# Kernel optimization log

Hardware: AMD Instinct MI355X
Metric: run time of the kernel (lower is better)

Reference implementation:

```python
import jax, jax.numpy as jnp
import numpy as np

B, T, H, W = 2, 4, 32, 32
DINO_DIM, COG_DIM, NUM_HEADS = 768, 1920, 12
HEAD_DIM = DINO_DIM // NUM_HEADS


def _layernorm(x, g, b, eps=1e-5):
    mu = jnp.mean(x, axis=-1, keepdims=True)
    var = jnp.mean(jnp.square(x - mu), axis=-1, keepdims=True)
    return (x - mu) * jax.lax.rsqrt(var + eps) * g + b


def setup_inputs() -> dict:
    key = jax.random.key(0)
    ks = jax.random.split(key, 12)
    s_d = 1.0 / np.sqrt(DINO_DIM)
    s_c = 1.0 / np.sqrt(COG_DIM)
    return {
        "dino_query": jax.random.normal(ks[0], (B, DINO_DIM, H, W), jnp.float32),
        "cogvideo_keys": jax.random.normal(ks[1], (B, T, H, W, COG_DIM), jnp.float32),
        "temporal_weights": jax.random.uniform(ks[2], (T,), jnp.float32),
        "Wq": jax.random.normal(ks[3], (DINO_DIM, DINO_DIM), jnp.float32) * s_d,
        "bq": jnp.zeros((DINO_DIM,), jnp.float32),
        "Wk": jax.random.normal(ks[4], (COG_DIM, DINO_DIM), jnp.float32) * s_c,
        "bk": jnp.zeros((DINO_DIM,), jnp.float32),
        "Wv": jax.random.normal(ks[5], (COG_DIM, DINO_DIM), jnp.float32) * s_c,
        "bv": jnp.zeros((DINO_DIM,), jnp.float32),
        "Wo": jax.random.normal(ks[6], (DINO_DIM, DINO_DIM), jnp.float32) * s_d,
        "bo": jnp.zeros((DINO_DIM,), jnp.float32),
        "gq": jnp.ones((DINO_DIM,), jnp.float32),
        "Bq": jnp.zeros((DINO_DIM,), jnp.float32),
        "gkv": jnp.ones((COG_DIM,), jnp.float32),
        "Bkv": jnp.zeros((COG_DIM,), jnp.float32),
    }


def reference(dino_query, cogvideo_keys, temporal_weights,
              Wq, bq, Wk, bk, Wv, bv, Wo, bo, gq, Bq, gkv, Bkv):
    b, c, h, w = dino_query.shape
    t = cogvideo_keys.shape[1]
    hw, tkv = h * w, t * cogvideo_keys.shape[2] * cogvideo_keys.shape[3]

    # [B,C,H,W] -> [B,H,W,C]; project after LayerNorm
    xq = _layernorm(jnp.transpose(dino_query, (0, 2, 3, 1)), gq, Bq)
    xkv = _layernorm(cogvideo_keys, gkv, Bkv)
    q = xq @ Wq + bq                      # [B,H,W,C]
    k = xkv @ Wk + bk                     # [B,T,Hk,Wk,C]
    v = xkv @ Wv + bv

    q = q.reshape(b, hw, NUM_HEADS, HEAD_DIM).transpose(0, 2, 1, 3)    # [B,nh,HW,hd]
    k = k.reshape(b, tkv, NUM_HEADS, HEAD_DIM).transpose(0, 2, 1, 3)   # [B,nh,TKV,hd]
    v = v.reshape(b, tkv, NUM_HEADS, HEAD_DIM).transpose(0, 2, 1, 3)

    scores = jnp.einsum('bnqd,bnkd->bnqk', q, k) / np.sqrt(HEAD_DIM)   # [B,nh,HW,TKV]
    # per-key temporal weight: each of the T frames contributes HW keys
    w_key = jnp.repeat(temporal_weights, tkv // t)                     # [TKV]
    scores = scores * w_key[None, None, None, :]
    probs = jax.nn.softmax(scores, axis=-1)

    out = jnp.einsum('bnqk,bnkd->bnqd', probs, v)                      # [B,nh,HW,hd]
    out = out.transpose(0, 2, 1, 3).reshape(b, h, w, c)
    out = out @ Wo + bo
    return jnp.transpose(out, (0, 3, 1, 2))                            # [B,C,H,W]
```

## Files before the change

### kernel.cpp

```cpp
#include <hip/hip_runtime.h>
#include <hip/hip_bf16.h>
#include <math.h>

#define BB   2
#define HWl  1024
#define DINO 768
#define COG  1920
#define NHh  12
#define TKV  4096
#define MQ   (BB*HWl)
#define MKV  (BB*TKV)
#define NSPL 4
#define ROWS_PER_SPLIT (BB*NHh*HWl)

typedef __attribute__((ext_vector_type(8))) short bf16x8;
typedef __attribute__((ext_vector_type(4))) float f32x4;

__device__ __forceinline__ unsigned short f2bf_bits(float f) {
    __hip_bfloat16 h = __float2bfloat16(f);
    return *reinterpret_cast<unsigned short*>(&h);
}

__device__ __forceinline__ void glds16(const __hip_bfloat16* g, __hip_bfloat16* l) {
    __builtin_amdgcn_global_load_lds((const __attribute__((address_space(1))) void*)g,
                                     (__attribute__((address_space(3))) void*)l, 16, 0, 0);
}

__global__ __launch_bounds__(256) void prep1(const float* __restrict__ dino,
                                             const float* __restrict__ cog,
                                             const float* __restrict__ gkv, const float* __restrict__ Bkv,
                                             const float* __restrict__ Wq, const float* __restrict__ Wk,
                                             const float* __restrict__ Wv, const float* __restrict__ Wo,
                                             float* __restrict__ xqT,
                                             __hip_bfloat16* __restrict__ xkv,
                                             __hip_bfloat16* WqT, __hip_bfloat16* WkvT, __hip_bfloat16* WoT) {
    int bid = blockIdx.x, tid = threadIdx.x;
    if (bid < 2048) {
        const int W = COG, W4 = W >> 2, NC = 8;
        int row = bid * 4 + (tid >> 6), lane = tid & 63;
        const float4* xr = (const float4*)(cog + (size_t)row * W);
        const float4* g4 = (const float4*)gkv;
        const float4* b4 = (const float4*)Bkv;
        float4 v[NC];
        float s = 0.f, ss = 0.f;
        #pragma unroll
        for (int i = 0; i < NC; ++i) {
            int c = lane + i * 64;
            float4 t = (c < W4) ? xr[c] : (float4){0.f, 0.f, 0.f, 0.f};
            v[i] = t;
            s  += t.x + t.y + t.z + t.w;
            ss += t.x * t.x + t.y * t.y + t.z * t.z + t.w * t.w;
        }
        #pragma unroll
        for (int off = 1; off < 64; off <<= 1) {
            s  += __shfl_xor(s, off);
            ss += __shfl_xor(ss, off);
        }
        float mu = s / W;
        float rstd = rsqrtf(ss / W - mu * mu + 1e-5f);
        ushort4* yr = (ushort4*)(xkv + (size_t)row * W);
        #pragma unroll
        for (int i = 0; i < NC; ++i) {
            int c = lane + i * 64;
            if (c < W4) {
                float4 t = v[i];
                float4 gg = g4[c], bb = b4[c];
                ushort4 o;
                o.x = f2bf_bits((t.x - mu) * rstd * gg.x + bb.x);
                o.y = f2bf_bits((t.y - mu) * rstd * gg.y + bb.y);
                o.z = f2bf_bits((t.z - mu) * rstd * gg.z + bb.z);
                o.w = f2bf_bits((t.w - mu) * rstd * gg.w + bb.w);
                yr[c] = o;
            }
        }
    } else if (bid < 2432) {
        int t = bid - 2048;
        int h0 = (t & 15) * 64;
        int c0 = ((t >> 4) % 12) * 64;
        int b = t / 192;
        __shared__ float T[64][65];
        #pragma unroll
        for (int i = 0; i < 16; ++i) {
            int idx = tid + i * 256;
            int c = idx >> 6, h = idx & 63;
            T[c][h] = dino[((size_t)b * DINO + c0 + c) * HWl + h0 + h];
        }
        __syncthreads();
        #pragma unroll
        for (int i = 0; i < 16; ++i) {
            int idx = tid + i * 256;
            int r = idx >> 6, c = idx & 63;
            xqT[((size_t)b * HWl + h0 + r) * DINO + c0 + c] = T[c][r];
        }
    } else {
        int bid2 = bid - 2432;
        int mid = bid2 / 1440, r = bid2 % 1440;
        int k0 = (r % 60) * 32, n0 = (r / 60) * 32;
        const float* src = (mid == 0) ? Wq : (mid == 1) ? Wk : (mid == 2) ? Wv : Wo;
        __hip_bfloat16* dst;
        int rowoff = 0;
        if (mid == 0) dst = WqT;
        else if (mid == 1) dst = WkvT;
        else if (mid == 2) { dst = WkvT; rowoff = 768; }
        else dst = WoT;
        int K = (mid == 1 || mid == 2) ? COG : DINO;
        if (k0 >= K) return;
        __shared__ float T[32][33];
        #pragma unroll
        for (int i = 0; i < 4; ++i) {
            int idx = tid + i * 256;
            int rr = idx >> 5, c = idx & 31;
            T[rr][c] = src[(size_t)(k0 + rr) * DINO + n0 + c];
        }
        __syncthreads();
        #pragma unroll
        for (int i = 0; i < 4; ++i) {
            int idx = tid + i * 256;
            int rr = idx >> 5, c = idx & 31;
            dst[(size_t)(rowoff + n0 + rr) * K + k0 + c] = __float2bfloat16(T[c][rr]);
        }
    }
}

__global__ __launch_bounds__(256) void prep2(const float* __restrict__ x,
                                             const float* __restrict__ g,
                                             const float* __restrict__ be,
                                             __hip_bfloat16* __restrict__ y) {
    const int W = DINO, NC = 3;
    int row = blockIdx.x * 4 + (threadIdx.x >> 6);
    int lane = threadIdx.x & 63;
    const float4* xr = (const float4*)(x + (size_t)row * W);
    const float4* g4 = (const float4*)g;
    const float4* b4 = (const float4*)be;
    float4 v[NC];
    float s = 0.f, ss = 0.f;
    #pragma unroll
    for (int i = 0; i < NC; ++i) {
        int c = lane + i * 64;
        float4 t = xr[c];
        v[i] = t;
        s  += t.x + t.y + t.z + t.w;
        ss += t.x * t.x + t.y * t.y + t.z * t.z + t.w * t.w;
    }
    #pragma unroll
    for (int off = 1; off < 64; off <<= 1) {
        s  += __shfl_xor(s, off);
        ss += __shfl_xor(ss, off);
    }
    float mu = s / W;
    float rstd = rsqrtf(ss / W - mu * mu + 1e-5f);
    ushort4* yr = (ushort4*)(y + (size_t)row * W);
    #pragma unroll
    for (int i = 0; i < NC; ++i) {
        int c = lane + i * 64;
        float4 t = v[i];
        float4 gg = g4[c], bb = b4[c];
        ushort4 o;
        o.x = f2bf_bits((t.x - mu) * rstd * gg.x + bb.x);
        o.y = f2bf_bits((t.y - mu) * rstd * gg.y + bb.y);
        o.z = f2bf_bits((t.z - mu) * rstd * gg.z + bb.z);
        o.w = f2bf_bits((t.w - mu) * rstd * gg.w + bb.w);
        yr[c] = o;
    }
}

#define VM6 asm volatile("s_waitcnt vmcnt(6)" ::: "memory")
#define VM2 asm volatile("s_waitcnt vmcnt(2)" ::: "memory")
#define VM0 asm volatile("s_waitcnt vmcnt(0)" ::: "memory")

#define STAGE_A(d, h, tau) do { \
    int _o = (aRow + (h) * 64) * Kd + (tau) * 64 + cgo; \
    __hip_bfloat16* _dp = SM + (d) * 32768 + (h) * 8192 + wido; \
    glds16(Ag + _o, _dp); \
    glds16(Ag + _o + 128 * Kd, _dp + 4096); \
} while (0)

#define STAGE_B(d, h, tau) do { \
    int _o = (bRow + (h) * 32) * Kd + (tau) * 64 + cgo; \
    __hip_bfloat16* _dp = SM + (d) * 32768 + 16384 + (h) * 8192 + wido; \
    glds16(Bg + _o, _dp); \
    glds16(Bg + _o + 128 * Kd, _dp + 4096); \
} while (0)

#define LDS_A_FRAG(dst, MH) do { \
    const __hip_bfloat16* _Ab = SM + cur * 32768 + (MH) * 8192 + aoff; \
    _Pragma("unroll") \
    for (int i = 0; i < 4; ++i) { \
        dst[i][0] = *(const bf16x8*)(_Ab + i * 1024 + c0); \
        dst[i][1] = *(const bf16x8*)(_Ab + i * 1024 + c1); \
    } \
} while (0)

#define LDS_B_FRAG(dst, NH) do { \
    const __hip_bfloat16* _Bb = SM + cur * 32768 + 16384 + (NH) * 8192 + boff; \
    _Pragma("unroll") \
    for (int j = 0; j < 2; ++j) { \
        dst[j][0] = *(const bf16x8*)(_Bb + j * 1024 + c0); \
        dst[j][1] = *(const bf16x8*)(_Bb + j * 1024 + c1); \
    } \
} while (0)

#define PHASE_MFMA(MH, af) do { \
    __builtin_amdgcn_sched_barrier(0); \
    __builtin_amdgcn_s_barrier(); \
    __builtin_amdgcn_sched_barrier(0); \
    __builtin_amdgcn_s_setprio(1); \
    _Pragma("unroll") \
    for (int i = 0; i < 4; ++i) \
        _Pragma("unroll") \
        for (int j = 0; j < 2; ++j) { \
            f32x4 _t = acc[(MH) * 4 + i][j]; \
            _t = __builtin_amdgcn_mfma_f32_16x16x32_bf16(af[i][0], b0[j][0], _t, 0, 0, 0); \
            _t = __builtin_amdgcn_mfma_f32_16x16x32_bf16(af[i][1], b0[j][1], _t, 0, 0, 0); \
            acc[(MH) * 4 + i][j] = _t; \
        } \
    _Pragma("unroll") \
    for (int i = 0; i < 4; ++i) \
        _Pragma("unroll") \
        for (int j = 0; j < 2; ++j) { \
            f32x4 _t = acc[(MH) * 4 + i][2 + j]; \
            _t = __builtin_amdgcn_mfma_f32_16x16x32_bf16(af[i][0], b1[j][0], _t, 0, 0, 0); \
            _t = __builtin_amdgcn_mfma_f32_16x16x32_bf16(af[i][1], b1[j][1], _t, 0, 0, 0); \
            acc[(MH) * 4 + i][2 + j] = _t; \
        } \
    __builtin_amdgcn_s_setprio(0); \
} while (0)

__global__ __launch_bounds__(512, 2) void stage1(const __hip_bfloat16* __restrict__ xq,
                                                 const __hip_bfloat16* __restrict__ WqT,
                                                 const float* __restrict__ bq,
                                                 __hip_bfloat16* __restrict__ qb,
                                                 const __hip_bfloat16* __restrict__ xkv,
                                                 const __hip_bfloat16* __restrict__ WkvT,
                                                 const float* __restrict__ bk,
                                                 const float* __restrict__ bv,
                                                 __hip_bfloat16* __restrict__ kb,
                                                 __hip_bfloat16* __restrict__ VT) {
    __shared__ __hip_bfloat16 SM[65536];
    int bid = blockIdx.x;
    int tid = threadIdx.x;
    int wid = tid >> 6, lane = tid & 63;
    int l4 = lane & 15, lq = lane >> 4;
    int wr = wid >> 2, wc = wid & 3;
    int tr = tid >> 3;
    int cgo = ((tid & 7) ^ (tr & 7)) * 8;
    int wido = wid * 512;

    const __hip_bfloat16 *Ag, *Bg;
    int m0, n0, Kd, NT, isQ;
    if (bid < 192) {
        int x = bid & 7, i = bid >> 3;
        m0 = (x * 4 + (i & 3)) * 256; n0 = (i >> 2) * 256;
        Ag = xkv; Bg = WkvT; Kd = COG; NT = COG / 64; isQ = 0;
    } else {
        int t = bid - 192;
        m0 = (t & 7) * 256; n0 = (t >> 3) * 256;
        Ag = xq; Bg = WqT; Kd = DINO; NT = DINO / 64; isQ = 1;
    }

    const int aRow = m0 + tr;
    const int bRow = n0 + ((tid >> 8) << 6) + (tr & 31);
    const int aoff = (wr * 64 + l4) * 64;
    const int boff = (wc * 32 + l4) * 64;
    const int c0 = ((lq) ^ (l4 & 7)) * 8;
    const int c1 = ((4 + lq) ^ (l4 & 7)) * 8;

    f32x4 acc[8][4];
    #pragma unroll
    for (int i = 0; i < 8; ++i)
        #pragma unroll
        for (int j = 0; j < 4; ++j) acc[i][j] = (f32x4){0.f, 0.f, 0.f, 0.f};

    bf16x8 a0[4][2], a1[4][2], b0[2][2], b1[2][2];

    STAGE_A(0, 0, 0); STAGE_B(0, 0, 0); STAGE_B(0, 1, 0); STAGE_A(0, 1, 0);
    VM2;
    __builtin_amdgcn_s_barrier();

    for (int g = 0; g < NT; ++g) {
        int cur = g & 1, nxt = cur ^ 1;
        bool s1 = (g + 1 < NT);
        LDS_A_FRAG(a0, 0);
        LDS_B_FRAG(b0, 0);
        LDS_B_FRAG(b1, 1);
        if (s1) { STAGE_A(nxt, 0, g + 1); STAGE_B(nxt, 0, g + 1); STAGE_B(nxt, 1, g + 1); VM6; }
        else VM0;
        PHASE_MFMA(0, a0);
        LDS_A_FRAG(a1, 1);
        if (s1) { STAGE_A(nxt, 1, g + 1); VM2; }
        PHASE_MFMA(1, a1);
    }

    if (isQ) {
        #pragma unroll
        for (int ii = 0; ii < 8; ++ii)
            #pragma unroll
            for (int jj = 0; jj < 4; ++jj) {
                int m = m0 + wr * 128 + (ii >> 2) * 64 + (ii & 3) * 16 + lq * 4;
                int n = n0 + wc * 64 + (jj >> 1) * 32 + (jj & 1) * 16 + l4;
                float bb = bq[n];
                #pragma unroll
                for (int r = 0; r < 4; ++r)
                    qb[(size_t)(m + r) * DINO + n] = __float2bfloat16(acc[ii][jj][r] + bb);
            }
    } else if (n0 < 768) {
        #pragma unroll
        for (int ii = 0; ii < 8; ++ii)
            #pragma unroll
            for (int jj = 0; jj < 4; ++jj) {
                int m = m0 + wr * 128 + (ii >> 2) * 64 + (ii & 3) * 16 + lq * 4;
                int n = n0 + wc * 64 + (jj >> 1) * 32 + (jj & 1) * 16 + l4;
                float bb = bk[n];
                #pragma unroll
                for (int r = 0; r < 4; ++r)
                    kb[(size_t)(m + r) * DINO + n] = __float2bfloat16(acc[ii][jj][r] + bb);
            }
    } else {
        #pragma unroll
        for (int ii = 0; ii < 8; ++ii)
            #pragma unroll
            for (int jj = 0; jj < 4; ++jj) {
                int m = m0 + wr * 128 + (ii >> 2) * 64 + (ii & 3) * 16 + lq * 4;
                int nv = n0 - 768 + wc * 64 + (jj >> 1) * 32 + (jj & 1) * 16 + l4;
                float bb = bv[nv];
                #pragma unroll
                for (int r = 0; r < 4; ++r) {
                    int mm = m + r;
                    VT[((size_t)((mm >> 12) * 768 + nv)) * TKV + (mm & 4095)] =
                        __float2bfloat16(acc[ii][jj][r] + bb);
                }
            }
    }
}

__global__ __launch_bounds__(256) void gemm_o(const __hip_bfloat16* __restrict__ A,
                                              const __hip_bfloat16* __restrict__ Bt,
                                              const float* __restrict__ bias,
                                              float* __restrict__ out) {
    const int K = DINO;
    __shared__ __hip_bfloat16 As[64 * 64];
    __shared__ __hip_bfloat16 Bs[64 * 64];
    int m0 = blockIdx.x * 64, n0 = blockIdx.y * 64;
    int tid = threadIdx.x, w = tid >> 6, lane = tid & 63;
    int l4 = lane & 15, lq = lane >> 4;
    int mq = (w & 1) * 32, nq = (w >> 1) * 32;
    f32x4 acc[2][2];
    #pragma unroll
    for (int i = 0; i < 2; ++i)
        #pragma unroll
        for (int j = 0; j < 2; ++j) acc[i][j] = (f32x4){0.f, 0.f, 0.f, 0.f};

    int rr = tid >> 3;
    int gc = (tid & 7) ^ (rr & 7);
    const __hip_bfloat16* ag = A  + (size_t)(m0 + rr) * K + gc * 8;
    const __hip_bfloat16* bg = Bt + (size_t)(n0 + rr) * K + gc * 8;
    __hip_bfloat16* asl = As + (w * 8) * 64;
    __hip_bfloat16* bsl = Bs + (w * 8) * 64;
    int sws = l4 & 7;

    for (int k0 = 0; k0 < K; k0 += 64) {
        __syncthreads();
        #pragma unroll
        for (int g = 0; g < 2; ++g) {
            glds16(ag + (size_t)(g * 32) * K + k0, asl + g * 32 * 64);
            glds16(bg + (size_t)(g * 32) * K + k0, bsl + g * 32 * 64);
        }
        __syncthreads();
        #pragma unroll
        for (int h = 0; h < 2; ++h) {
            bf16x8 a[2], b[2];
            #pragma unroll
            for (int i = 0; i < 2; ++i)
                a[i] = *(const bf16x8*)(As + (mq + 16 * i + l4) * 64 + (((h * 4 + lq) ^ sws) * 8));
            #pragma unroll
            for (int j = 0; j < 2; ++j)
                b[j] = *(const bf16x8*)(Bs + (nq + 16 * j + l4) * 64 + (((h * 4 + lq) ^ sws) * 8));
            #pragma unroll
            for (int i = 0; i < 2; ++i)
                #pragma unroll
                for (int j = 0; j < 2; ++j)
                    acc[i][j] = __builtin_amdgcn_mfma_f32_16x16x32_bf16(b[j], a[i], acc[i][j], 0, 0, 0);
        }
    }
    #pragma unroll
    for (int i = 0; i < 2; ++i)
        #pragma unroll
        for (int j = 0; j < 2; ++j)
            #pragma unroll
            for (int r = 0; r < 4; ++r) {
                int n = n0 + nq + 16 * j + lq * 4 + r;
                int m = m0 + mq + 16 * i + l4;
                int b = m >> 10, hw = m & 1023;
                out[((size_t)b * DINO + n) * HWl + hw] = acc[i][j][r] + bias[n];
            }
}

__global__ __launch_bounds__(256) void attn4(const __hip_bfloat16* __restrict__ qb,
                                             const __hip_bfloat16* __restrict__ kb,
                                             const __hip_bfloat16* __restrict__ VT,
                                             const float* __restrict__ tw,
                                             __hip_bfloat16* __restrict__ Opart,
                                             float* __restrict__ lpart) {
    int bid = blockIdx.x;
    int g = bid % 96, qc = bid / 96;
    int s = g & 3, bh = g >> 2;
    int head = bh % NHh, b = bh / NHh;
    int tid = threadIdx.x, w = tid >> 6, lane = tid & 63;
    int l4 = lane & 15, lq = lane >> 4;

    __shared__ __hip_bfloat16 Ks[2 * 64 * 64];
    __shared__ __hip_bfloat16 Vs[2 * 64 * 64];
    __shared__ __hip_bfloat16 Ps[4 * 32 * 64];

    const __hip_bfloat16* qbase = qb + (size_t)(b * HWl + qc * 128 + w * 32 + l4) * DINO + head * 64;
    bf16x8 qA0 = *(const bf16x8*)(qbase + lq * 8);
    bf16x8 qA1 = *(const bf16x8*)(qbase + 32 + lq * 8);
    const __hip_bfloat16* qbase2 = qbase + (size_t)16 * DINO;
    bf16x8 qB0 = *(const bf16x8*)(qbase2 + lq * 8);
    bf16x8 qB1 = *(const bf16x8*)(qbase2 + 32 + lq * 8);

    float c = tw[s] * 0.125f * 1.44269504f;
    float l_iA = 0.f, l_iB = 0.f;
    f32x4 oA[4], oB[4];
    #pragma unroll
    for (int j = 0; j < 4; ++j) { oA[j] = (f32x4){0.f,0.f,0.f,0.f}; oB[j] = (f32x4){0.f,0.f,0.f,0.f}; }

    int rowA = w * 16 + (lane >> 3);
    int cg = (lane & 7) ^ ((lane >> 3) & 7);
    const __hip_bfloat16* kg0 = kb + (size_t)(b * TKV + s * 1024 + rowA) * DINO + head * 64 + cg * 8;
    const __hip_bfloat16* kg1 = kg0 + (size_t)8 * DINO;
    const __hip_bfloat16* vg0 = VT + (size_t)(b * 768 + head * 64 + rowA) * TKV + s * 1024 + cg * 8;
    const __hip_bfloat16* vg1 = vg0 + (size_t)8 * TKV;
    int klo0 = (w * 2 + 0) * 512, klo1 = (w * 2 + 1) * 512;

    int sw0 = (lq ^ (l4 & 7)) * 8;
    int sw1 = ((4 + lq) ^ (l4 & 7)) * 8;
    __hip_bfloat16* PsA = Ps + w * 2048 + l4 * 64;
    __hip_bfloat16* PsB = Ps + w * 2048 + (16 + l4) * 64;

    glds16(kg0, Ks + klo0);
    glds16(kg1, Ks + klo1);
    glds16(vg0, Vs + klo0);
    glds16(vg1, Vs + klo1);

    for (int kt = 0; kt < 16; ++kt) {
        int cur = (kt & 1) * 4096;
        __syncthreads();
        if (kt < 15) {
            int nxt = cur ^ 4096;
            glds16(kg0 + (size_t)(kt + 1) * 64 * DINO, Ks + nxt + klo0);
            glds16(kg1 + (size_t)(kt + 1) * 64 * DINO, Ks + nxt + klo1);
            glds16(vg0 + (kt + 1) * 64, Vs + nxt + klo0);
            glds16(vg1 + (kt + 1) * 64, Vs + nxt + klo1);
        }
        const __hip_bfloat16* Kc = Ks + cur;
        const __hip_bfloat16* Vc = Vs + cur;

        f32x4 stA[4], stB[4];
        #pragma unroll
        for (int j = 0; j < 4; ++j) {
            const __hip_bfloat16* kr = Kc + (16 * j + l4) * 64;
            bf16x8 kf0 = *(const bf16x8*)(kr + sw0);
            bf16x8 kf1 = *(const bf16x8*)(kr + sw1);
            f32x4 a = (f32x4){0.f,0.f,0.f,0.f};
            a = __builtin_amdgcn_mfma_f32_16x16x32_bf16(kf0, qA0, a, 0, 0, 0);
            a = __builtin_amdgcn_mfma_f32_16x16x32_bf16(kf1, qA1, a, 0, 0, 0);
            stA[j] = a;
            f32x4 bb = (f32x4){0.f,0.f,0.f,0.f};
            bb = __builtin_amdgcn_mfma_f32_16x16x32_bf16(kf0, qB0, bb, 0, 0, 0);
            bb = __builtin_amdgcn_mfma_f32_16x16x32_bf16(kf1, qB1, bb, 0, 0, 0);
            stB[j] = bb;
        }

        float lsA = 0.f, lsB = 0.f;
        #pragma unroll
        for (int j = 0; j < 4; ++j)
            #pragma unroll
            for (int r = 0; r < 4; ++r) {
                float eA = exp2f(stA[j][r] * c);
                float eB = exp2f(stB[j][r] * c);
                stA[j][r] = eA; lsA += eA;
                stB[j][r] = eB; lsB += eB;
            }
        lsA += __shfl_xor(lsA, 16); lsA += __shfl_xor(lsA, 32);
        lsB += __shfl_xor(lsB, 16); lsB += __shfl_xor(lsB, 32);
        l_iA += lsA; l_iB += lsB;

        #pragma unroll
        for (int j = 0; j < 4; ++j) {
            int off = (((2 * j + (lq >> 1)) ^ (l4 & 7)) << 3) + (lq & 1) * 4;
            ushort4 pA, pB;
            pA.x = f2bf_bits(stA[j][0]); pA.y = f2bf_bits(stA[j][1]);
            pA.z = f2bf_bits(stA[j][2]); pA.w = f2bf_bits(stA[j][3]);
            pB.x = f2bf_bits(stB[j][0]); pB.y = f2bf_bits(stB[j][1]);
            pB.z = f2bf_bits(stB[j][2]); pB.w = f2bf_bits(stB[j][3]);
            *(ushort4*)&PsA[off] = pA;
            *(ushort4*)&PsB[off] = pB;
        }
        bf16x8 paA0 = *(const bf16x8*)(PsA + sw0);
        bf16x8 paA1 = *(const bf16x8*)(PsA + sw1);
        bf16x8 paB0 = *(const bf16x8*)(PsB + sw0);
        bf16x8 paB1 = *(const bf16x8*)(PsB + sw1);

        #pragma unroll
        for (int j = 0; j < 4; ++j) {
            const __hip_bfloat16* vr = Vc + (16 * j + l4) * 64;
            bf16x8 vf0 = *(const bf16x8*)(vr + sw0);
            bf16x8 vf1 = *(const bf16x8*)(vr + sw1);
            oA[j] = __builtin_amdgcn_mfma_f32_16x16x32_bf16(paA0, vf0, oA[j], 0, 0, 0);
            oA[j] = __builtin_amdgcn_mfma_f32_16x16x32_bf16(paA1, vf1, oA[j], 0, 0, 0);
            oB[j] = __builtin_amdgcn_mfma_f32_16x16x32_bf16(paB0, vf0, oB[j], 0, 0, 0);
            oB[j] = __builtin_amdgcn_mfma_f32_16x16x32_bf16(paB1, vf1, oB[j], 0, 0, 0);
        }
    }

    size_t rb = (size_t)s * ROWS_PER_SPLIT + (size_t)(b * NHh + head) * HWl + qc * 128 + w * 32;
    #pragma unroll
    for (int j = 0; j < 4; ++j)
        #pragma unroll
        for (int r = 0; r < 4; ++r) {
            Opart[(rb + lq * 4 + r) * 64 + j * 16 + l4]      = __float2bfloat16(oA[j][r]);
            Opart[(rb + 16 + lq * 4 + r) * 64 + j * 16 + l4] = __float2bfloat16(oB[j][r]);
        }
    if (lq == 0) {
        lpart[rb + l4]      = l_iA;
        lpart[rb + 16 + l4] = l_iB;
    }
}

__global__ void combine(const __hip_bfloat16* __restrict__ Opart, const float* __restrict__ lpart,
                        __hip_bfloat16* __restrict__ attn) {
    int p = blockIdx.x * 4 + (threadIdx.x >> 6);
    int d = threadIdx.x & 63;
    float L = 0.f, O = 0.f;
    #pragma unroll
    for (int s = 0; s < NSPL; ++s) {
        L += lpart[(size_t)s * ROWS_PER_SPLIT + p];
        O += __bfloat162float(Opart[((size_t)s * ROWS_PER_SPLIT + p) * 64 + d]);
    }
    float res = O / L;
    int q = p & 1023;
    int bh = p >> 10;
    int head = bh % NHh, b = bh / NHh;
    attn[((size_t)(b * HWl + q)) * DINO + head * 64 + d] = __float2bfloat16(res);
}

extern "C" void kernel_launch(void* const* d_in, const int* in_sizes, int n_in,
                              void* d_out, int out_size, void* d_ws, size_t ws_size,
                              hipStream_t stream) {
    (void)in_sizes; (void)n_in; (void)out_size; (void)ws_size;
    const float* dino = (const float*)d_in[0];
    const float* cog  = (const float*)d_in[1];
    const float* tw   = (const float*)d_in[2];
    const float* Wq   = (const float*)d_in[3];
    const float* bq   = (const float*)d_in[4];
    const float* Wk   = (const float*)d_in[5];
    const float* bk   = (const float*)d_in[6];
    const float* Wv   = (const float*)d_in[7];
    const float* bv   = (const float*)d_in[8];
    const float* Wo   = (const float*)d_in[9];
    const float* bo   = (const float*)d_in[10];
    const float* gq   = (const float*)d_in[11];
    const float* Bq   = (const float*)d_in[12];
    const float* gkv  = (const float*)d_in[13];
    const float* Bkv  = (const float*)d_in[14];

    char* p = (char*)d_ws;
    float* xqT = (float*)p;                    p += (size_t)MQ * DINO * 4;
    __hip_bfloat16* xq = (__hip_bfloat16*)p;   p += (size_t)MQ * DINO * 2;
    char* alias = p;                           p += (size_t)MKV * COG * 2;
    __hip_bfloat16* xkv = (__hip_bfloat16*)alias;
    __hip_bfloat16* WqT  = (__hip_bfloat16*)p; p += (size_t)DINO * DINO * 2;
    __hip_bfloat16* WkvT = (__hip_bfloat16*)p; p += (size_t)1536 * COG * 2;
    __hip_bfloat16* WoT  = (__hip_bfloat16*)p; p += (size_t)DINO * DINO * 2;
    __hip_bfloat16* qb   = (__hip_bfloat16*)p; p += (size_t)MQ  * DINO * 2;
    __hip_bfloat16* kb   = (__hip_bfloat16*)p; p += (size_t)MKV * DINO * 2;
    __hip_bfloat16* VT   = (__hip_bfloat16*)p; p += (size_t)MKV * DINO * 2;
    __hip_bfloat16* attnb = (__hip_bfloat16*)p; p += (size_t)MQ * DINO * 2;
    __hip_bfloat16* Opart = (__hip_bfloat16*)alias;
    float* lpart = (float*)(alias + (size_t)NSPL * ROWS_PER_SPLIT * 64 * 2);

    prep1<<<8192, 256, 0, stream>>>(dino, cog, gkv, Bkv,
                                    Wq, Wk, Wv, Wo, xqT, xkv, WqT, WkvT, WoT);
    prep2<<<MQ / 4, 256, 0, stream>>>(xqT, gq, Bq, xq);
    stage1<<<216, 512, 0, stream>>>(xq, WqT, bq, qb, xkv, WkvT, bk, bv, kb, VT);
    attn4<<<BB * NHh * 8 * NSPL, 256, 0, stream>>>(qb, kb, VT, tw, Opart, lpart);
    combine<<<ROWS_PER_SPLIT / 4, 256, 0, stream>>>(Opart, lpart, attnb);
    gemm_o<<<dim3(32, 12), 256, 0, stream>>>(attnb, WoT, bo, (float*)d_out);
}
```

Measured before the change: 255.5 us.

## Issue next-tile loads before barrier and vectorize V-transpose stores

Reorders the double-buffered GEMM main loop so the global-to-LDS prefetch for the next K tile is issued at the top of each iteration, before the barrier and fragment reads. The waitcnt threshold rises from 6 to 8 to match, which keeps more loads in flight and hides load latency behind the MFMAs. The V output epilogue also packs four consecutive bf16 values into one 8-byte store instead of four scalar strided stores. The reordered waits and barriers carry a risk of LDS hazards if the counts are off.

```diff
diff --git a/kernel.cpp b/kernel.cpp
--- a/kernel.cpp
+++ b/kernel.cpp
@@ -164,9 +164,10 @@
     }
 }
 
-#define VM6 asm volatile("s_waitcnt vmcnt(6)" ::: "memory")
+#define VM8 asm volatile("s_waitcnt vmcnt(8)" ::: "memory")
 #define VM2 asm volatile("s_waitcnt vmcnt(2)" ::: "memory")
 #define VM0 asm volatile("s_waitcnt vmcnt(0)" ::: "memory")
+#define SBAR0 __builtin_amdgcn_sched_barrier(0)
 
 #define STAGE_A(d, h, tau) do { \
     int _o = (aRow + (h) * 64) * Kd + (tau) * 64 + cgo; \
@@ -200,10 +201,7 @@
     } \
 } while (0)
 
-#define PHASE_MFMA(MH, af) do { \
-    __builtin_amdgcn_sched_barrier(0); \
-    __builtin_amdgcn_s_barrier(); \
-    __builtin_amdgcn_sched_barrier(0); \
+#define MFMA_HALF(MH, af) do { \
     __builtin_amdgcn_s_setprio(1); \
     _Pragma("unroll") \
     for (int i = 0; i < 4; ++i) \
@@ -274,21 +272,22 @@
     bf16x8 a0[4][2], a1[4][2], b0[2][2], b1[2][2];
 
     STAGE_A(0, 0, 0); STAGE_B(0, 0, 0); STAGE_B(0, 1, 0); STAGE_A(0, 1, 0);
-    VM2;
-    __builtin_amdgcn_s_barrier();
 
     for (int g = 0; g < NT; ++g) {
         int cur = g & 1, nxt = cur ^ 1;
         bool s1 = (g + 1 < NT);
+        if (s1) { STAGE_A(nxt, 0, g + 1); STAGE_B(nxt, 0, g + 1); STAGE_B(nxt, 1, g + 1); VM8; }
+        else VM2;
+        SBAR0; __builtin_amdgcn_s_barrier(); SBAR0;
         LDS_A_FRAG(a0, 0);
         LDS_B_FRAG(b0, 0);
         LDS_B_FRAG(b1, 1);
-        if (s1) { STAGE_A(nxt, 0, g + 1); STAGE_B(nxt, 0, g + 1); STAGE_B(nxt, 1, g + 1); VM6; }
+        MFMA_HALF(0, a0);
+        if (s1) { STAGE_A(nxt, 1, g + 1); VM8; }
         else VM0;
-        PHASE_MFMA(0, a0);
+        SBAR0; __builtin_amdgcn_s_barrier(); SBAR0;
         LDS_A_FRAG(a1, 1);
-        if (s1) { STAGE_A(nxt, 1, g + 1); VM2; }
-        PHASE_MFMA(1, a1);
+        MFMA_HALF(1, a1);
     }
 
     if (isQ) {
@@ -323,12 +322,12 @@
                 int m = m0 + wr * 128 + (ii >> 2) * 64 + (ii & 3) * 16 + lq * 4;
                 int nv = n0 - 768 + wc * 64 + (jj >> 1) * 32 + (jj & 1) * 16 + l4;
                 float bb = bv[nv];
-                #pragma unroll
-                for (int r = 0; r < 4; ++r) {
-                    int mm = m + r;
-                    VT[((size_t)((mm >> 12) * 768 + nv)) * TKV + (mm & 4095)] =
-                        __float2bfloat16(acc[ii][jj][r] + bb);
-                }
+                ushort4 pk;
+                pk.x = f2bf_bits(acc[ii][jj][0] + bb);
+                pk.y = f2bf_bits(acc[ii][jj][1] + bb);
+                pk.z = f2bf_bits(acc[ii][jj][2] + bb);
+                pk.w = f2bf_bits(acc[ii][jj][3] + bb);
+                *(ushort4*)&VT[((size_t)((m >> 12) * 768 + nv)) * TKV + (m & 4095)] = pk;
             }
     }
 }
```

After: 255.6 us. No clear change (+0.0%).
